# Optimization experiments

Hardware: AMD Instinct MI355X
Metric: run time of the kernel (lower is better)

## Reference

```python
import jax, jax.numpy as jnp
import numpy as np

B, N, F = 1024, 784, 1
C1, C2, H, NCLS = 32, 32, 512, 10


def setup_inputs() -> dict:
    key = jax.random.key(0)
    ks = jax.random.split(key, 10)
    x = jax.random.normal(ks[0], (B, N, F), jnp.float32)
    # dense (renormalized-style) adjacency, shared across the batch; rows roughly sum to ~1
    a = jax.random.uniform(ks[1], (N, N), jnp.float32) * (2.0 / N)
    def glorot(k, shape):
        lim = np.sqrt(6.0 / (shape[0] + shape[1])).astype(np.float32)
        return jax.random.uniform(k, shape, jnp.float32, -lim, lim)
    return {
        "x": x,
        "a": a,
        "w1": glorot(ks[2], (F, C1)),
        "b1": jnp.zeros((C1,), jnp.float32),
        "w2": glorot(ks[3], (C1, C2)),
        "b2": jnp.zeros((C2,), jnp.float32),
        "wf1": glorot(ks[4], (N * C2, H)),
        "bf1": jnp.zeros((H,), jnp.float32),
        "wf2": glorot(ks[5], (H, NCLS)),
        "bf2": jnp.zeros((NCLS,), jnp.float32),
    }


def _graph_conv(x, a, w, b):
    # Spektral GraphConv (batch mode): elu(A @ (X @ W) + b)
    xw = jnp.einsum('bnf,fc->bnc', x, w)
    agg = jnp.einsum('nm,bmc->bnc', a, xw)
    return jax.nn.elu(agg + b)


def reference(x, a, w1, b1, w2, b2, wf1, bf1, wf2, bf2):
    h = _graph_conv(x, a, w1, b1)          # [B, N, 32]
    h = _graph_conv(h, a, w2, b2)          # [B, N, 32]
    h = h.reshape(h.shape[0], -1)          # Flatten -> [B, N*32]
    h = jax.nn.relu(h @ wf1 + bf1)         # [B, 512]
    return jax.nn.softmax(h @ wf2 + bf2, axis=-1)  # [B, 10]
```

## Files before the change

kernel.cpp:

```cpp
#include <hip/hip_runtime.h>
#include <hip/hip_bf16.h>
#include <math.h>

#define BATCH 1024
#define NREAL 784
#define NPAD  896
#define C1D   32
#define C2D   32
#define HDIM  512
#define NCLS  10
#define KFC   25088

#define KS_G1 7
#define KS_FC 14

#define BM 128
#define BN 128
#define BK 32

using bf16x8  = __attribute__((ext_vector_type(8))) __bf16;
using floatx4 = __attribute__((ext_vector_type(4))) float;

__device__ __forceinline__ float elu_f(float t) {
    return t > 0.f ? t : (__expf(t) - 1.f);
}

__device__ __forceinline__ void wg_barrier_lds() {
    asm volatile("s_waitcnt lgkmcnt(0)\n\ts_barrier" ::: "memory");
}

__device__ __forceinline__ void bar() {
    asm volatile("s_barrier" ::: "memory");
}

__device__ __forceinline__ void lgkm0_fence() {
    asm volatile("s_waitcnt lgkmcnt(0)" ::: "memory");
    __builtin_amdgcn_sched_barrier(0);
}

__device__ __forceinline__ void gload_lds16(const __hip_bfloat16* g, __hip_bfloat16* l) {
    __builtin_amdgcn_global_load_lds(
        (const __attribute__((address_space(1))) void*)g,
        (__attribute__((address_space(3))) void*)l, 16, 0, 0);
}

template<int MODE>
__launch_bounds__(256)
__global__ void gemm_bt(const __hip_bfloat16* __restrict__ A, int lda,
                        const __hip_bfloat16* __restrict__ Bm, int ldb,
                        int kIters, int kPerZ, size_t sliceStride,
                        float* __restrict__ outF, int ldc,
                        __hip_bfloat16* __restrict__ outH,
                        const float* __restrict__ bias)
{
    __shared__ __align__(16) __hip_bfloat16 As[2][BM * BK];
    __shared__ __align__(16) __hip_bfloat16 Bs[2][BN * BK];

    const int tid  = threadIdx.x;
    const int lane = tid & 63;
    const int wave = tid >> 6;
    const int wi = wave >> 1, wj = wave & 1;

    const int m0 = blockIdx.y * BM;
    const int n0 = blockIdx.x * BN;
    const int kBase = blockIdx.z * kPerZ;

    const int rowInChunk = lane >> 2;
    const int kOff8 = (lane & 3) * 8;

    const __hip_bfloat16* aSrc0 = A  + (size_t)(m0 + (wave * 2 + 0) * 16 + rowInChunk) * lda + kBase + kOff8;
    const __hip_bfloat16* aSrc1 = A  + (size_t)(m0 + (wave * 2 + 1) * 16 + rowInChunk) * lda + kBase + kOff8;
    const __hip_bfloat16* bSrc0 = Bm + (size_t)(n0 + (wave * 2 + 0) * 16 + rowInChunk) * ldb + kBase + kOff8;
    const __hip_bfloat16* bSrc1 = Bm + (size_t)(n0 + (wave * 2 + 1) * 16 + rowInChunk) * ldb + kBase + kOff8;

    const int wSlot = (((lane & 3) + ((lane >> 3) & 3)) & 3) * 8;
    const int ldsW0 = (wave * 2 + 0) * 512 + rowInChunk * 32 + wSlot;
    const int ldsW1 = ldsW0 + 512;

    const int rSlot = ((((lane >> 4) + (((lane & 15) >> 1) & 3)) & 3)) * 8;
    const int rRow  = lane & 15;

    floatx4 acc[4][4];
    const floatx4 zero4 = {0.f, 0.f, 0.f, 0.f};
    #pragma unroll
    for (int i = 0; i < 4; i++)
        #pragma unroll
        for (int j = 0; j < 4; j++) acc[i][j] = zero4;

    int4 aA0, aA1, bA0, bA1;
    int4 aB0, aB1, bB0, bB1;

    aA0 = *(const int4*)aSrc0; aA1 = *(const int4*)aSrc1;
    bA0 = *(const int4*)bSrc0; bA1 = *(const int4*)bSrc1;
    aSrc0 += BK; aSrc1 += BK; bSrc0 += BK; bSrc1 += BK;
    aB0 = *(const int4*)aSrc0; aB1 = *(const int4*)aSrc1;
    bB0 = *(const int4*)bSrc0; bB1 = *(const int4*)bSrc1;
    aSrc0 += BK; aSrc1 += BK; bSrc0 += BK; bSrc1 += BK;

    *(int4*)(&As[0][ldsW0]) = aA0;
    *(int4*)(&As[0][ldsW1]) = aA1;
    *(int4*)(&Bs[0][ldsW0]) = bA0;
    *(int4*)(&Bs[0][ldsW1]) = bA1;
    wg_barrier_lds();

    for (int kt = 0; kt < kIters; kt += 2) {
        const bool more = (kt + 2 < kIters);

        {
            bf16x8 af[4], bfr[4];
            #pragma unroll
            for (int mi = 0; mi < 4; mi++)
                af[mi] = *(const bf16x8*)(&As[0][(wi * 64 + mi * 16 + rRow) * BK + rSlot]);
            #pragma unroll
            for (int nj = 0; nj < 4; nj++)
                bfr[nj] = *(const bf16x8*)(&Bs[0][(wj * 64 + nj * 16 + rRow) * BK + rSlot]);

            if (more) {
                aA0 = *(const int4*)aSrc0; aA1 = *(const int4*)aSrc1;
                bA0 = *(const int4*)bSrc0; bA1 = *(const int4*)bSrc1;
                aSrc0 += BK; aSrc1 += BK; bSrc0 += BK; bSrc1 += BK;
            }
            *(int4*)(&As[1][ldsW0]) = aB0;
            *(int4*)(&As[1][ldsW1]) = aB1;
            *(int4*)(&Bs[1][ldsW0]) = bB0;
            *(int4*)(&Bs[1][ldsW1]) = bB1;

            #pragma unroll
            for (int mi = 0; mi < 4; mi++)
                #pragma unroll
                for (int nj = 0; nj < 4; nj++)
                    acc[mi][nj] = __builtin_amdgcn_mfma_f32_16x16x32_bf16(af[mi], bfr[nj], acc[mi][nj], 0, 0, 0);

            wg_barrier_lds();
        }

        {
            bf16x8 af[4], bfr[4];
            #pragma unroll
            for (int mi = 0; mi < 4; mi++)
                af[mi] = *(const bf16x8*)(&As[1][(wi * 64 + mi * 16 + rRow) * BK + rSlot]);
            #pragma unroll
            for (int nj = 0; nj < 4; nj++)
                bfr[nj] = *(const bf16x8*)(&Bs[1][(wj * 64 + nj * 16 + rRow) * BK + rSlot]);

            if (more) {
                aB0 = *(const int4*)aSrc0; aB1 = *(const int4*)aSrc1;
                bB0 = *(const int4*)bSrc0; bB1 = *(const int4*)bSrc1;
                aSrc0 += BK; aSrc1 += BK; bSrc0 += BK; bSrc1 += BK;
                *(int4*)(&As[0][ldsW0]) = aA0;
                *(int4*)(&As[0][ldsW1]) = aA1;
                *(int4*)(&Bs[0][ldsW0]) = bA0;
                *(int4*)(&Bs[0][ldsW1]) = bA1;
            }

            #pragma unroll
            for (int mi = 0; mi < 4; mi++)
                #pragma unroll
                for (int nj = 0; nj < 4; nj++)
                    acc[mi][nj] = __builtin_amdgcn_mfma_f32_16x16x32_bf16(af[mi], bfr[nj], acc[mi][nj], 0, 0, 0);

            wg_barrier_lds();
        }
    }

    #pragma unroll
    for (int mi = 0; mi < 4; mi++) {
        #pragma unroll
        for (int nj = 0; nj < 4; nj++) {
            #pragma unroll
            for (int r = 0; r < 4; r++) {
                const int row = m0 + wi * 64 + mi * 16 + (lane >> 4) * 4 + r;
                const int col = n0 + wj * 64 + nj * 16 + (lane & 15);
                const float v = acc[mi][nj][r];
                if (MODE == 1) {
                    if (row < NREAL) {
                        const int c = col & 31, b = col >> 5;
                        const float t = elu_f(v + bias[c]);
                        outH[(size_t)b * KFC + row * 32 + c] = __float2bfloat16(t);
                    }
                } else {
                    outF[(size_t)blockIdx.z * sliceStride + (size_t)row * ldc + col] = v;
                }
            }
        }
    }
}

#define KT_G3 14

#define STAGE_A(tt, hh) do {                                                    \
    const int s_ = (2 * (tt) + (hh)) & 3;                                       \
    gload_lds16(aSrcH[hh][0] + (tt) * 64, &Ah[s_][(wave * 2 + 0) * 512]);       \
    gload_lds16(aSrcH[hh][1] + (tt) * 64, &Ah[s_][(wave * 2 + 1) * 512]);       \
} while (0)

#define STAGE_B(tt, hh) do {                                                    \
    const int s_ = (2 * (tt) + (hh)) & 3;                                       \
    gload_lds16(bSrcH[hh][0] + (tt) * 64, &Bh[s_][(wave * 2 + 0) * 512]);       \
    gload_lds16(bSrcH[hh][1] + (tt) * 64, &Bh[s_][(wave * 2 + 1) * 512]);       \
} while (0)

#define G3_PHASE(QM, QN, ISS)                                                   \
  {                                                                             \
    const int sA_ = (2 * t + (QM)) & 3;                                         \
    const int sB_ = (2 * t + (QN)) & 3;                                         \
    bf16x8 a0_[4], a1_[4], b0_[2], b1_[2];                                      \
    _Pragma("unroll")                                                           \
    for (int mi_ = 0; mi_ < 4; mi_++) {                                         \
      const int ro_ = aBase + mi_ * 1024;                                       \
      a0_[mi_] = *(const bf16x8*)(&Ah[sA_][ro_ + koff0]);                       \
      a1_[mi_] = *(const bf16x8*)(&Ah[sA_][ro_ + koff1]);                       \
    }                                                                           \
    _Pragma("unroll")                                                           \
    for (int nj_ = 0; nj_ < 2; nj_++) {                                         \
      const int ro_ = bBase + nj_ * 1024;                                       \
      b0_[nj_] = *(const bf16x8*)(&Bh[sB_][ro_ + koff0]);                       \
      b1_[nj_] = *(const bf16x8*)(&Bh[sB_][ro_ + koff1]);                       \
    }                                                                           \
    ISS                                                                         \
    lgkm0_fence();                                                              \
    __builtin_amdgcn_s_setprio(1);                                              \
    _Pragma("unroll")                                                           \
    for (int nj_ = 0; nj_ < 2; nj_++)                                           \
      _Pragma("unroll")                                                         \
      for (int mi_ = 0; mi_ < 4; mi_++)                                         \
        acc[(QM) * 2 + (QN)][mi_][nj_] = __builtin_amdgcn_mfma_f32_16x16x32_bf16( \
            a0_[mi_], b0_[nj_], acc[(QM) * 2 + (QN)][mi_][nj_], 0, 0, 0);       \
    _Pragma("unroll")                                                           \
    for (int nj_ = 0; nj_ < 2; nj_++)                                           \
      _Pragma("unroll")                                                         \
      for (int mi_ = 0; mi_ < 4; mi_++)                                         \
        acc[(QM) * 2 + (QN)][mi_][nj_] = __builtin_amdgcn_mfma_f32_16x16x32_bf16( \
            a1_[mi_], b1_[nj_], acc[(QM) * 2 + (QN)][mi_][nj_], 0, 0, 0);       \
    __builtin_amdgcn_s_setprio(0);                                              \
  }

__launch_bounds__(512, 2)
__global__ void gemm256_g3(const __hip_bfloat16* __restrict__ Ag,
                           const __hip_bfloat16* __restrict__ Bg,
                           __hip_bfloat16* __restrict__ outH,
                           const float* __restrict__ bias)
{
    __shared__ __align__(16) __hip_bfloat16 Ah[4][128 * 64];
    __shared__ __align__(16) __hip_bfloat16 Bh[4][128 * 64];

    const int tid  = threadIdx.x;
    const int lane = tid & 63;
    const int wave = tid >> 6;
    const int vm = wave >> 2, vn = wave & 3;

    const int mR = blockIdx.y * 256;
    const int nR = blockIdx.x * 256;

    const int rRow = lane & 15;
    const int gHi  = lane >> 4;
    const int rot  = lane & 7;
    const int koff0 = (((gHi + rot) & 7) << 3);
    const int koff1 = ((((4 + gHi) + rot) & 7) << 3);
    const int aBase = (vm * 64 + rRow) * 64;
    const int bBase = (vn * 32 + rRow) * 64;

    const int rowLoc = lane >> 3;
    const int gOff   = ((((lane & 7) - rowLoc) & 7) << 3);
    const __hip_bfloat16* aSrcH[2][2];
    const __hip_bfloat16* bSrcH[2][2];
    #pragma unroll
    for (int h = 0; h < 2; h++)
        #pragma unroll
        for (int j = 0; j < 2; j++) {
            int ra = mR + h * 128 + (wave * 2 + j) * 8 + rowLoc;
            if (ra > NPAD - 1) ra = NPAD - 1;
            aSrcH[h][j] = Ag + (size_t)ra * NPAD + gOff;
            const int rb = nR + h * 128 + (wave * 2 + j) * 8 + rowLoc;
            bSrcH[h][j] = Bg + (size_t)rb * NPAD + gOff;
        }

    const float bias0 = bias[rRow];
    const float bias1 = bias[16 + rRow];

    floatx4 acc[4][4][2];
    const floatx4 zero4 = {0.f, 0.f, 0.f, 0.f};
    #pragma unroll
    for (int q = 0; q < 4; q++)
        #pragma unroll
        for (int i = 0; i < 4; i++)
            #pragma unroll
            for (int j = 0; j < 2; j++) acc[q][i][j] = zero4;

    STAGE_A(0, 0);
    STAGE_A(0, 1); STAGE_B(0, 1); STAGE_B(0, 0);
    STAGE_A(1, 0);

    #pragma unroll 2
    for (int t = 0; t < KT_G3; ++t) {
        if (t == KT_G3 - 1) { asm volatile("s_waitcnt vmcnt(0)" ::: "memory"); }
        else                { asm volatile("s_waitcnt vmcnt(2)" ::: "memory"); }
        bar();

        G3_PHASE(0, 0, {
            if (t + 1 < KT_G3) { STAGE_A(t + 1, 1); STAGE_B(t + 1, 1); STAGE_B(t + 1, 0); }
        })
        G3_PHASE(0, 1, { })

        bar();

        G3_PHASE(1, 0, {
            if (t + 2 < KT_G3) { STAGE_A(t + 2, 0); }
        })
        G3_PHASE(1, 1, { })
    }

    #pragma unroll
    for (int q = 0; q < 4; q++) {
        const int qm = q >> 1, qn = q & 1;
        #pragma unroll
        for (int mi = 0; mi < 4; mi++) {
            #pragma unroll
            for (int nj = 0; nj < 2; nj++) {
                #pragma unroll
                for (int r = 0; r < 4; r++) {
                    const int row = mR + qm * 128 + vm * 64 + mi * 16 + gHi * 4 + r;
                    if (row < NREAL) {
                        const int col = nR + qn * 128 + vn * 32 + nj * 16 + rRow;
                        const int c = col & 31, b = col >> 5;
                        const float bv = nj ? bias1 : bias0;
                        const float v = elu_f(acc[q][mi][nj][r] + bv);
                        outH[(size_t)b * KFC + row * 32 + c] = __float2bfloat16(v);
                    }
                }
            }
        }
    }
}

__global__ void convX(const float* __restrict__ x, __hip_bfloat16* __restrict__ Xbf) {
    const int idx = blockIdx.x * 256 + threadIdx.x;
    if (idx >= BATCH * NPAD) return;
    const int m = idx % NPAD, b = idx / NPAD;
    const float v = (m < NREAL) ? x[(size_t)b * NREAL + m] : 0.f;
    Xbf[idx] = __float2bfloat16(v);
}

__global__ void convA(const float* __restrict__ a, __hip_bfloat16* __restrict__ Abf) {
    const int idx = blockIdx.x * 256 + threadIdx.x;
    if (idx >= NPAD * NPAD) return;
    const int m = idx % NPAD, n = idx / NPAD;
    const float v = (m < NREAL && n < NREAL) ? a[(size_t)n * NREAL + m] : 0.f;
    Abf[idx] = __float2bfloat16(v);
}

__global__ void convW(const float* __restrict__ wf1, __hip_bfloat16* __restrict__ Wt) {
    __shared__ float tile[32][33];
    const int k0 = blockIdx.x * 32, h0 = blockIdx.y * 32;
    const int tx = threadIdx.x, ty = threadIdx.y;
    #pragma unroll
    for (int i = 0; i < 4; i++)
        tile[ty * 4 + i][tx] = wf1[(size_t)(k0 + ty * 4 + i) * HDIM + h0 + tx];
    __syncthreads();
    #pragma unroll
    for (int i = 0; i < 4; i++)
        Wt[(size_t)(h0 + ty * 4 + i) * KFC + k0 + tx] = __float2bfloat16(tile[tx][ty * 4 + i]);
}

__global__ void layer1_fuse(const float* __restrict__ Ypart,
                            const float* __restrict__ w1, const float* __restrict__ b1,
                            const float* __restrict__ w2,
                            __hip_bfloat16* __restrict__ Tt)
{
    __shared__ __align__(16) float sW2[C1D * C2D];
    __shared__ float sw1[C1D], sb1[C1D];
    const int tid = threadIdx.x;
    for (int i = tid; i < C1D * C2D; i += 128) sW2[i] = w2[i];
    if (tid < C1D) { sw1[tid] = w1[tid]; sb1[tid] = b1[tid]; }
    __syncthreads();

    const int m = blockIdx.x * 128 + tid;
    const int b = blockIdx.y;
    float y = 0.f;
    #pragma unroll
    for (int z = 0; z < KS_G1; z++)
        y += Ypart[(size_t)z * (BATCH * NPAD) + (size_t)b * NPAD + m];

    float h[C1D];
    #pragma unroll
    for (int c1 = 0; c1 < C1D; c1++) h[c1] = elu_f(y * sw1[c1] + sb1[c1]);

    float4 t4[8];
    #pragma unroll
    for (int q = 0; q < 8; q++) t4[q] = make_float4(0.f, 0.f, 0.f, 0.f);
    #pragma unroll
    for (int c1 = 0; c1 < C1D; c1++) {
        const float hv = h[c1];
        const float4* row = (const float4*)(sW2 + c1 * C2D);
        #pragma unroll
        for (int q = 0; q < 8; q++) {
            const float4 w = row[q];
            t4[q].x += hv * w.x; t4[q].y += hv * w.y;
            t4[q].z += hv * w.z; t4[q].w += hv * w.w;
        }
    }
    const float* tf = (const float*)t4;
    #pragma unroll
    for (int c = 0; c < C2D; c++)
        Tt[((size_t)(b * 32 + c)) * NPAD + m] = __float2bfloat16(tf[c]);
}

__global__ void fc2_softmax(const float* __restrict__ part, const float* __restrict__ bf1,
                            const float* __restrict__ wf2, const float* __restrict__ bf2,
                            float* __restrict__ out)
{
    __shared__ float sW[HDIM * NCLS];
    __shared__ float sb[NCLS];
    const int tid = threadIdx.x;
    for (int i = tid; i < HDIM * NCLS; i += 256) sW[i] = wf2[i];
    if (tid < NCLS) sb[tid] = bf2[tid];
    __syncthreads();

    const int lane = tid & 63, wave = tid >> 6;
    const int b = blockIdx.x * 4 + wave;

    float acc[NCLS];
    #pragma unroll
    for (int c = 0; c < NCLS; c++) acc[c] = 0.f;
    #pragma unroll
    for (int q = 0; q < 8; q++) {
        const int h = q * 64 + lane;
        float hv = bf1[h];
        #pragma unroll
        for (int z = 0; z < KS_FC; z++)
            hv += part[(size_t)z * (BATCH * HDIM) + (size_t)b * HDIM + h];
        hv = hv > 0.f ? hv : 0.f;
        #pragma unroll
        for (int c = 0; c < NCLS; c++) acc[c] += hv * sW[h * NCLS + c];
    }
    #pragma unroll
    for (int c = 0; c < NCLS; c++) {
        #pragma unroll
        for (int off = 32; off >= 1; off >>= 1) acc[c] += __shfl_down(acc[c], off);
    }
    if (lane == 0) {
        float mx = -1e30f;
        #pragma unroll
        for (int c = 0; c < NCLS; c++) { acc[c] += sb[c]; mx = fmaxf(mx, acc[c]); }
        float e[NCLS], s = 0.f;
        #pragma unroll
        for (int c = 0; c < NCLS; c++) { e[c] = __expf(acc[c] - mx); s += e[c]; }
        const float inv = 1.f / s;
        #pragma unroll
        for (int c = 0; c < NCLS; c++) out[(size_t)b * NCLS + c] = e[c] * inv;
    }
}

extern "C" void kernel_launch(void* const* d_in, const int* in_sizes, int n_in,
                              void* d_out, int out_size, void* d_ws, size_t ws_size,
                              hipStream_t stream)
{
    const float* x   = (const float*)d_in[0];
    const float* a   = (const float*)d_in[1];
    const float* w1  = (const float*)d_in[2];
    const float* b1  = (const float*)d_in[3];
    const float* w2  = (const float*)d_in[4];
    const float* b2  = (const float*)d_in[5];
    const float* wf1 = (const float*)d_in[6];
    const float* bf1 = (const float*)d_in[7];
    const float* wf2 = (const float*)d_in[8];
    const float* bf2 = (const float*)d_in[9];
    float* out = (float*)d_out;

    char* ws = (char*)d_ws;
    __hip_bfloat16* h2f  = (__hip_bfloat16*)(ws + 0);
    float*          Ypart= (float*)(ws + 0);
    __hip_bfloat16* Tt   = (__hip_bfloat16*)(ws + 51380224);
    __hip_bfloat16* Wt   = (__hip_bfloat16*)(ws + 51380224);
    float*          part = (float*)(ws + 77070336);
    __hip_bfloat16* Abf  = (__hip_bfloat16*)(ws + 110100480);
    __hip_bfloat16* Xbf  = (__hip_bfloat16*)(ws + 111706112);

    convX<<<(BATCH * NPAD + 255) / 256, 256, 0, stream>>>(x, Xbf);
    convA<<<(NPAD * NPAD + 255) / 256, 256, 0, stream>>>(a, Abf);

    gemm_bt<2><<<dim3(NPAD / BN, BATCH / BM, KS_G1), 256, 0, stream>>>(
        Xbf, NPAD, Abf, NPAD, (NPAD / KS_G1) / BK, NPAD / KS_G1,
        (size_t)BATCH * NPAD, Ypart, NPAD, nullptr, nullptr);

    layer1_fuse<<<dim3(NPAD / 128, BATCH), 128, 0, stream>>>(Ypart, w1, b1, w2, Tt);

    gemm256_g3<<<dim3(BATCH * 32 / 256, 1024 / 256), 512, 0, stream>>>(Abf, Tt, h2f, b2);

    convW<<<dim3(KFC / 32, HDIM / 32), dim3(32, 8), 0, stream>>>(wf1, Wt);

    gemm_bt<2><<<dim3(HDIM / BN, BATCH / BM, KS_FC), 256, 0, stream>>>(
        h2f, KFC, Wt, KFC, (KFC / KS_FC) / BK, KFC / KS_FC,
        (size_t)BATCH * HDIM, part, HDIM, nullptr, nullptr);

    fc2_softmax<<<BATCH / 4, 256, 0, stream>>>(part, bf1, wf2, bf2, out);
}
```

Before: 280.1 us.

## Enlarge per-wave MFMA tile to 128x64 and simplify prefetch pipeline

The graph-conv GEMM kernel now gives each wave one 128x64 output tile instead of four 64x32 quadrants. This raises MFMA count per LDS fragment load (16 MFMAs per 8 fragment loads instead of 8 per 6). The two-deep staggered prefetch with partial vmcnt waits and two barriers per iteration is replaced by a single-stage-ahead prefetch, interleaved with the MFMA groups, behind one barrier and a full vmcnt(0) wait. The explicit lgkmcnt fences go away, so LDS wait placement is left to the compiler. The shallower pipeline risks exposing global-load latency.

```diff
diff --git a/kernel.cpp b/kernel.cpp
--- a/kernel.cpp
+++ b/kernel.cpp
@@ -31,11 +31,6 @@
 
 __device__ __forceinline__ void bar() {
     asm volatile("s_barrier" ::: "memory");
-}
-
-__device__ __forceinline__ void lgkm0_fence() {
-    asm volatile("s_waitcnt lgkmcnt(0)" ::: "memory");
-    __builtin_amdgcn_sched_barrier(0);
 }
 
 __device__ __forceinline__ void gload_lds16(const __hip_bfloat16* g, __hip_bfloat16* l) {
@@ -200,41 +195,6 @@
     gload_lds16(bSrcH[hh][1] + (tt) * 64, &Bh[s_][(wave * 2 + 1) * 512]);       \
 } while (0)
 
-#define G3_PHASE(QM, QN, ISS)                                                   \
-  {                                                                             \
-    const int sA_ = (2 * t + (QM)) & 3;                                         \
-    const int sB_ = (2 * t + (QN)) & 3;                                         \
-    bf16x8 a0_[4], a1_[4], b0_[2], b1_[2];                                      \
-    _Pragma("unroll")                                                           \
-    for (int mi_ = 0; mi_ < 4; mi_++) {                                         \
-      const int ro_ = aBase + mi_ * 1024;                                       \
-      a0_[mi_] = *(const bf16x8*)(&Ah[sA_][ro_ + koff0]);                       \
-      a1_[mi_] = *(const bf16x8*)(&Ah[sA_][ro_ + koff1]);                       \
-    }                                                                           \
-    _Pragma("unroll")                                                           \
-    for (int nj_ = 0; nj_ < 2; nj_++) {                                         \
-      const int ro_ = bBase + nj_ * 1024;                                       \
-      b0_[nj_] = *(const bf16x8*)(&Bh[sB_][ro_ + koff0]);                       \
-      b1_[nj_] = *(const bf16x8*)(&Bh[sB_][ro_ + koff1]);                       \
-    }                                                                           \
-    ISS                                                                         \
-    lgkm0_fence();                                                              \
-    __builtin_amdgcn_s_setprio(1);                                              \
-    _Pragma("unroll")                                                           \
-    for (int nj_ = 0; nj_ < 2; nj_++)                                           \
-      _Pragma("unroll")                                                         \
-      for (int mi_ = 0; mi_ < 4; mi_++)                                         \
-        acc[(QM) * 2 + (QN)][mi_][nj_] = __builtin_amdgcn_mfma_f32_16x16x32_bf16( \
-            a0_[mi_], b0_[nj_], acc[(QM) * 2 + (QN)][mi_][nj_], 0, 0, 0);       \
-    _Pragma("unroll")                                                           \
-    for (int nj_ = 0; nj_ < 2; nj_++)                                           \
-      _Pragma("unroll")                                                         \
-      for (int mi_ = 0; mi_ < 4; mi_++)                                         \
-        acc[(QM) * 2 + (QN)][mi_][nj_] = __builtin_amdgcn_mfma_f32_16x16x32_bf16( \
-            a1_[mi_], b1_[nj_], acc[(QM) * 2 + (QN)][mi_][nj_], 0, 0, 0);       \
-    __builtin_amdgcn_s_setprio(0);                                              \
-  }
-
 __launch_bounds__(512, 2)
 __global__ void gemm256_g3(const __hip_bfloat16* __restrict__ Ag,
                            const __hip_bfloat16* __restrict__ Bg,
@@ -248,6 +208,7 @@
     const int lane = tid & 63;
     const int wave = tid >> 6;
     const int vm = wave >> 2, vn = wave & 3;
+    const int hbB = vn >> 1;
 
     const int mR = blockIdx.y * 256;
     const int nR = blockIdx.x * 256;
@@ -256,9 +217,9 @@
     const int gHi  = lane >> 4;
     const int rot  = lane & 7;
     const int koff0 = (((gHi + rot) & 7) << 3);
-    const int koff1 = ((((4 + gHi) + rot) & 7) << 3);
-    const int aBase = (vm * 64 + rRow) * 64;
-    const int bBase = (vn * 32 + rRow) * 64;
+    const int koff1 = ((((gHi + 4) + rot) & 7) << 3);
+    const int aRow0 = rRow * 64;
+    const int bRow0 = ((vn & 1) * 64 + rRow) * 64;
 
     const int rowLoc = lane >> 3;
     const int gOff   = ((((lane & 7) - rowLoc) & 7) << 3);
@@ -278,55 +239,88 @@
     const float bias0 = bias[rRow];
     const float bias1 = bias[16 + rRow];
 
-    floatx4 acc[4][4][2];
+    floatx4 acc[8][4];
     const floatx4 zero4 = {0.f, 0.f, 0.f, 0.f};
     #pragma unroll
-    for (int q = 0; q < 4; q++)
-        #pragma unroll
-        for (int i = 0; i < 4; i++)
-            #pragma unroll
-            for (int j = 0; j < 2; j++) acc[q][i][j] = zero4;
-
-    STAGE_A(0, 0);
-    STAGE_A(0, 1); STAGE_B(0, 1); STAGE_B(0, 0);
-    STAGE_A(1, 0);
+    for (int i = 0; i < 8; i++)
+        #pragma unroll
+        for (int j = 0; j < 4; j++) acc[i][j] = zero4;
+
+    STAGE_A(0, 0); STAGE_A(0, 1);
+    STAGE_B(0, 0); STAGE_B(0, 1);
 
     #pragma unroll 2
     for (int t = 0; t < KT_G3; ++t) {
-        if (t == KT_G3 - 1) { asm volatile("s_waitcnt vmcnt(0)" ::: "memory"); }
-        else                { asm volatile("s_waitcnt vmcnt(2)" ::: "memory"); }
+        asm volatile("s_waitcnt vmcnt(0)" ::: "memory");
         bar();
 
-        G3_PHASE(0, 0, {
-            if (t + 1 < KT_G3) { STAGE_A(t + 1, 1); STAGE_B(t + 1, 1); STAGE_B(t + 1, 0); }
-        })
-        G3_PHASE(0, 1, { })
-
-        bar();
-
-        G3_PHASE(1, 0, {
-            if (t + 2 < KT_G3) { STAGE_A(t + 2, 0); }
-        })
-        G3_PHASE(1, 1, { })
-    }
-
-    #pragma unroll
-    for (int q = 0; q < 4; q++) {
-        const int qm = q >> 1, qn = q & 1;
-        #pragma unroll
-        for (int mi = 0; mi < 4; mi++) {
-            #pragma unroll
-            for (int nj = 0; nj < 2; nj++) {
-                #pragma unroll
-                for (int r = 0; r < 4; r++) {
-                    const int row = mR + qm * 128 + vm * 64 + mi * 16 + gHi * 4 + r;
-                    if (row < NREAL) {
-                        const int col = nR + qn * 128 + vn * 32 + nj * 16 + rRow;
-                        const int c = col & 31, b = col >> 5;
-                        const float bv = nj ? bias1 : bias0;
-                        const float v = elu_f(acc[q][mi][nj][r] + bv);
-                        outH[(size_t)b * KFC + row * 32 + c] = __float2bfloat16(v);
-                    }
+        const int sA = (2 * t + vm)  & 3;
+        const int sB = (2 * t + hbB) & 3;
+        const __hip_bfloat16* Ab = &Ah[sA][aRow0];
+        const __hip_bfloat16* Bb = &Bh[sB][bRow0];
+
+        bf16x8 a_[4], b_[4];
+
+        #pragma unroll
+        for (int nj = 0; nj < 4; nj++) b_[nj] = *(const bf16x8*)(Bb + nj * 1024 + koff0);
+        #pragma unroll
+        for (int mi = 0; mi < 4; mi++) a_[mi] = *(const bf16x8*)(Ab + mi * 1024 + koff0);
+        if (t + 1 < KT_G3) { STAGE_A(t + 1, 0); STAGE_A(t + 1, 1); }
+        __builtin_amdgcn_s_setprio(1);
+        #pragma unroll
+        for (int mi = 0; mi < 4; mi++)
+            #pragma unroll
+            for (int nj = 0; nj < 4; nj++)
+                acc[mi][nj] = __builtin_amdgcn_mfma_f32_16x16x32_bf16(a_[mi], b_[nj], acc[mi][nj], 0, 0, 0);
+        __builtin_amdgcn_s_setprio(0);
+
+        #pragma unroll
+        for (int mi = 0; mi < 4; mi++) a_[mi] = *(const bf16x8*)(Ab + (4 + mi) * 1024 + koff0);
+        if (t + 1 < KT_G3) { STAGE_B(t + 1, 0); STAGE_B(t + 1, 1); }
+        __builtin_amdgcn_s_setprio(1);
+        #pragma unroll
+        for (int mi = 0; mi < 4; mi++)
+            #pragma unroll
+            for (int nj = 0; nj < 4; nj++)
+                acc[4 + mi][nj] = __builtin_amdgcn_mfma_f32_16x16x32_bf16(a_[mi], b_[nj], acc[4 + mi][nj], 0, 0, 0);
+        __builtin_amdgcn_s_setprio(0);
+
+        #pragma unroll
+        for (int nj = 0; nj < 4; nj++) b_[nj] = *(const bf16x8*)(Bb + nj * 1024 + koff1);
+        #pragma unroll
+        for (int mi = 0; mi < 4; mi++) a_[mi] = *(const bf16x8*)(Ab + mi * 1024 + koff1);
+        __builtin_amdgcn_s_setprio(1);
+        #pragma unroll
+        for (int mi = 0; mi < 4; mi++)
+            #pragma unroll
+            for (int nj = 0; nj < 4; nj++)
+                acc[mi][nj] = __builtin_amdgcn_mfma_f32_16x16x32_bf16(a_[mi], b_[nj], acc[mi][nj], 0, 0, 0);
+        __builtin_amdgcn_s_setprio(0);
+
+        #pragma unroll
+        for (int mi = 0; mi < 4; mi++) a_[mi] = *(const bf16x8*)(Ab + (4 + mi) * 1024 + koff1);
+        __builtin_amdgcn_s_setprio(1);
+        #pragma unroll
+        for (int mi = 0; mi < 4; mi++)
+            #pragma unroll
+            for (int nj = 0; nj < 4; nj++)
+                acc[4 + mi][nj] = __builtin_amdgcn_mfma_f32_16x16x32_bf16(a_[mi], b_[nj], acc[4 + mi][nj], 0, 0, 0);
+        __builtin_amdgcn_s_setprio(0);
+    }
+
+    #pragma unroll
+    for (int mi = 0; mi < 8; mi++) {
+        #pragma unroll
+        for (int nj = 0; nj < 4; nj++) {
+            #pragma unroll
+            for (int r = 0; r < 4; r++) {
+                const int row = mR + vm * 128 + mi * 16 + gHi * 4 + r;
+                if (row < NREAL) {
+                    const int col = nR + vn * 64 + nj * 16 + rRow;
+                    const int c = col & 31, b = col >> 5;
+                    const float bv = (nj & 1) ? bias1 : bias0;
+                    const float v = elu_f(acc[mi][nj][r] + bv);
+                    outH[(size_t)b * KFC + row * 32 + c] = __float2bfloat16(v);
                 }
             }
         }
```

Result: slower. 295.7 us (+5.6%).
